# Kernel tuning notes

Hardware: AMD Instinct MI355X
Metric: run time of the kernel (lower is better)

The kernel has to match this reference:

```python
import jax, jax.numpy as jnp
import numpy as np

NEG_SLOPE = 0.2

def gat_layer(x, src, dst, W, a_src, a_dst, num_nodes):
    """PyG-style GATConv. W:[F_in,H*C], a_src/a_dst:[H,C]. Returns [N,H,C]."""
    H, C = a_src.shape
    h = (x @ W).reshape(num_nodes, H, C)                      # [N,H,C]
    e_src = jnp.sum(h * a_src, axis=-1)                       # [N,H]
    e_dst = jnp.sum(h * a_dst, axis=-1)                       # [N,H]
    e = jax.nn.leaky_relu(e_src[src] + e_dst[dst], NEG_SLOPE) # [E,H]
    # segment softmax over incoming edges of each destination node
    m = jax.ops.segment_max(e, dst, num_segments=num_nodes)
    w = jnp.exp(e - m[dst])
    z = jax.ops.segment_sum(w, dst, num_segments=num_nodes)
    alpha = w / (z[dst] + 1e-16)                               # [E,H]
    msg = h[src] * alpha[:, :, None]                           # [E,H,C]
    return jax.ops.segment_sum(msg, dst, num_segments=num_nodes)


def setup_inputs() -> dict:
    key = jax.random.key(0)
    ks = jax.random.split(key, 16)
    N, E, F_IN, HID, A, G = 50000, 800000, 128, 128, 32, 64
    x = jax.random.normal(ks[0], (N, F_IN), dtype=jnp.float32)
    edge_index = jax.random.randint(ks[1], (2, E), 0, N, dtype=jnp.int32)
    batch = jnp.sort(jax.random.randint(ks[2], (N,), 0, G, dtype=jnp.int32))
    s = 0.1
    W1 = jax.random.normal(ks[3], (F_IN, 2 * HID), jnp.float32) * s
    a_src1 = jax.random.normal(ks[4], (2, HID), jnp.float32) * s
    a_dst1 = jax.random.normal(ks[5], (2, HID), jnp.float32) * s
    b1 = jnp.zeros((2 * HID,), jnp.float32)
    W2 = jax.random.normal(ks[6], (2 * HID, HID), jnp.float32) * s
    a_src2 = jax.random.normal(ks[7], (1, HID), jnp.float32) * s
    a_dst2 = jax.random.normal(ks[8], (1, HID), jnp.float32) * s
    b2 = jnp.zeros((HID,), jnp.float32)
    Wp = jax.random.normal(ks[9], (HID, A), jnp.float32) * s
    bp = jnp.zeros((A,), jnp.float32)
    Wv = jax.random.normal(ks[10], (HID, 1), jnp.float32) * s
    bv = jnp.zeros((1,), jnp.float32)
    return {"x": x, "edge_index": edge_index, "batch": batch,
            "W1": W1, "a_src1": a_src1, "a_dst1": a_dst1, "b1": b1,
            "W2": W2, "a_src2": a_src2, "a_dst2": a_dst2, "b2": b2,
            "Wp": Wp, "bp": bp, "Wv": Wv, "bv": bv}


def reference(x, edge_index, batch, W1, a_src1, a_dst1, b1,
              W2, a_src2, a_dst2, b2, Wp, bp, Wv, bv):
    N = x.shape[0]
    G = 64  # number of graphs in the batch
    # add self-loops (PyG GATConv default)
    loop = jnp.arange(N, dtype=edge_index.dtype)
    src = jnp.concatenate([edge_index[0], loop])
    dst = jnp.concatenate([edge_index[1], loop])
    # layer 1: heads=2, concat=True
    h1 = gat_layer(x, src, dst, W1, a_src1, a_dst1, N)        # [N,2,HID]
    h1 = jax.nn.elu(h1.reshape(N, -1) + b1)                   # [N,2*HID]
    # layer 2: heads=1, concat=False (mean over heads = identity for H=1)
    h2 = gat_layer(h1, src, dst, W2, a_src2, a_dst2, N)       # [N,1,HID]
    h2 = jax.nn.elu(h2.reshape(N, -1) + b2)                   # [N,HID]
    # global mean pool over graphs
    sums = jax.ops.segment_sum(h2, batch, num_segments=G)
    cnt = jax.ops.segment_sum(jnp.ones((N,), h2.dtype), batch, num_segments=G)
    x_pool = sums / jnp.maximum(cnt, 1.0)[:, None]            # [G,HID]
    policy_logits = x_pool @ Wp + bp                          # [G,A]
    state_value = x_pool @ Wv + bv                            # [G,1]
    return (policy_logits, state_value)
```

## Files before the change

kernel.cpp:

```cpp
#include <hip/hip_runtime.h>
#include <hip/hip_bf16.h>
#include <cstdint>


typedef __attribute__((ext_vector_type(8))) short bf16x8;
typedef __attribute__((ext_vector_type(4))) float f32x4;

#define RANGES 8

__device__ __forceinline__ float wave_sum(float v) {
#pragma unroll
    for (int off = 32; off >= 1; off >>= 1) v += __shfl_xor(v, off, 64);
    return v;
}

__device__ __forceinline__ unsigned short f2bf(float f) {
    union { float f; uint32_t u; } c; c.f = f;
    uint32_t u = c.u;
    return (unsigned short)((u + 0x7fffu + ((u >> 16) & 1u)) >> 16);
}

__device__ __forceinline__ float bf2f(unsigned short u) {
    union { uint32_t u; float f; } c; c.u = ((uint32_t)u) << 16;
    return c.f;
}


template <int K, int FOUT>
__device__ __forceinline__ void swizzle_body(const float* __restrict__ W, int ldW, int colOff,
                                             unsigned short* __restrict__ Bsw, int tid) {
    constexpr int CPW = FOUT / 4, NCT = CPW / 16, KST = K / 32;
    if (tid >= K * FOUT / 8) return;
    int lane = tid & 63;
    int rest = tid >> 6;
    int t = rest % KST; rest /= KST;
    int c = rest % NCT; rest /= NCT;
    int cg_ = rest;
    int quad = lane >> 4, lo = lane & 15;
    int col = colOff + cg_ * CPW + c * 16 + lo;
    unsigned short v[8];
#pragma unroll
    for (int j = 0; j < 8; ++j)
        v[j] = f2bf(W[(t * 32 + quad * 8 + j) * ldW + col]);
    ushort4* dst = (ushort4*)(Bsw + (size_t)tid * 8);
    ushort4 o0, o1;
    o0.x = v[0]; o0.y = v[1]; o0.z = v[2]; o0.w = v[3];
    o1.x = v[4]; o1.y = v[5]; o1.z = v[6]; o1.w = v[7];
    dst[0] = o0; dst[1] = o1;
}


__global__ void init_kernel(const float* __restrict__ W1, const float* __restrict__ W2,
                            const float* __restrict__ a_src1, const float* __restrict__ a_dst1,
                            unsigned short* __restrict__ B1h0, unsigned short* __restrict__ B1h1,
                            unsigned short* __restrict__ B2,
                            float* __restrict__ v1s, float* __restrict__ v1d,
                            int* __restrict__ zbase, int zn4) {
    int b = blockIdx.x;
    if (b < 8)        swizzle_body<128, 128>(W1, 256, 0,   B1h0, b * 256 + threadIdx.x);
    else if (b < 16)  swizzle_body<128, 128>(W1, 256, 128, B1h1, (b - 8) * 256 + threadIdx.x);
    else if (b < 32)  swizzle_body<256, 128>(W2, 128, 0,   B2, (b - 16) * 256 + threadIdx.x);
    else if (b == 32) {
        int t = threadIdx.x, h = t >> 7, k = t & 127;
        float vs = 0.f, vd = 0.f;
        for (int c = 0; c < 128; ++c) {
            float w = W1[k * 256 + h * 128 + c];
            vs += w * a_src1[h * 128 + c];
            vd += w * a_dst1[h * 128 + c];
        }
        v1s[h * 128 + k] = vs;
        v1d[h * 128 + k] = vd;
    } else {
        int i = (b - 33) * 256 + threadIdx.x;
        if (i < zn4) ((int4*)zbase)[i] = make_int4(0, 0, 0, 0);
    }
}


__global__ void degree_kernel(const int* __restrict__ ei, int* __restrict__ deg,
                              int* __restrict__ eoff, int E, int N) {
    int i = blockIdx.x * blockDim.x + threadIdx.x;
    if (i >= E + N) return;
    int dst = (i < E) ? ei[E + i] : (i - E);
    eoff[i] = atomicAdd(&deg[dst], 1);
}

__global__ __launch_bounds__(256) void scan_tiles(int* __restrict__ deg,
                                                  int* __restrict__ tsum, int N) {
    __shared__ int buf[256];
    const int t = threadIdx.x;
    const int base = blockIdx.x * 1024 + t * 4;
    int v[4]; int s = 0;
#pragma unroll
    for (int k = 0; k < 4; ++k) { v[k] = (base + k < N) ? deg[base + k] : 0; s += v[k]; }
    buf[t] = s;
    __syncthreads();
#pragma unroll
    for (int off = 1; off < 256; off <<= 1) {
        int x = (t >= off) ? buf[t - off] : 0;
        __syncthreads();
        buf[t] += x;
        __syncthreads();
    }
    int run = buf[t] - s;
#pragma unroll
    for (int k = 0; k < 4; ++k) {
        if (base + k < N) deg[base + k] = run;
        run += v[k];
    }
    if (t == 255) tsum[blockIdx.x] = buf[255];
}

__global__ __launch_bounds__(256) void scan_add(const int* __restrict__ partial,
                                                const int* __restrict__ tsum,
                                                int* __restrict__ rowptr, int N, int T) {
    __shared__ int s_toff;
    const int tile = blockIdx.x;
    if (threadIdx.x < 64) {
        int t = threadIdx.x;
        int v = (t < T) ? tsum[t] : 0;
#pragma unroll
        for (int off = 1; off < 64; off <<= 1) {
            int x = __shfl_up(v, off, 64);
            if (t >= off) v += x;
        }
        int toff = (tile == 0) ? 0 : __shfl(v, tile - 1, 64);
        if (t == 0) s_toff = toff;
        if (tile == 0 && t == 63) rowptr[N] = v;
    }
    __syncthreads();
    const int toff = s_toff;
    int i = tile * 1024 + threadIdx.x * 4;
#pragma unroll
    for (int k = 0; k < 4; ++k) {
        if (i + k < N) rowptr[i + k] = partial[i + k] + toff;
    }
}

__global__ void scatter_kernel(const int* __restrict__ ei, const int* __restrict__ eoff,
                               const int* __restrict__ rowptr, int* __restrict__ csr_src,
                               int E, int N, int SBLK, int RSIZE) {
    int r = blockIdx.x / SBLK;
    int i = (blockIdx.x % SBLK) * 256 + threadIdx.x;
    if (i >= E + N) return;
    int dst = (i < E) ? ei[E + i] : (i - E);
    int lo = r * RSIZE;
    if (dst < lo || dst >= lo + RSIZE) return;
    int src = (i < E) ? ei[i] : dst;
    csr_src[rowptr[dst] + eoff[i]] = src;
}


__global__ void attn1_cast(const float* __restrict__ x, const float* __restrict__ v1s,
                           const float* __restrict__ v1d, float* __restrict__ es1,
                           float* __restrict__ ed1, unsigned short* __restrict__ xbf, int N) {
    int wid = (blockIdx.x * blockDim.x + threadIdx.x) >> 6;
    int lane = threadIdx.x & 63;
    if (wid >= N) return;
    float2 xv = *(const float2*)(x + (size_t)wid * 128 + lane * 2);
    float p0s = xv.x * v1s[lane * 2] + xv.y * v1s[lane * 2 + 1];
    float p1s = xv.x * v1s[128 + lane * 2] + xv.y * v1s[128 + lane * 2 + 1];
    float p0d = xv.x * v1d[lane * 2] + xv.y * v1d[lane * 2 + 1];
    float p1d = xv.x * v1d[128 + lane * 2] + xv.y * v1d[128 + lane * 2 + 1];
    p0s = wave_sum(p0s); p1s = wave_sum(p1s);
    p0d = wave_sum(p0d); p1d = wave_sum(p1d);
    if (lane == 0) {
        es1[wid * 2] = p0s; es1[wid * 2 + 1] = p1s;
        ed1[wid * 2] = p0d; ed1[wid * 2 + 1] = p1d;
    }
    ushort2 o; o.x = f2bf(xv.x); o.y = f2bf(xv.y);
    *(ushort2*)(xbf + (size_t)wid * 128 + lane * 2) = o;
}


__global__ void gat_agg_x(const unsigned short* __restrict__ xbf,
                          const float* __restrict__ es, const float* __restrict__ ed,
                          const int* __restrict__ rowptr, const int* __restrict__ csr_src,
                          unsigned short* __restrict__ aggx, int N, int NPAD) {
    __shared__ float w_lds[4][2][32];
    __shared__ int   s_lds[4][32];
    int wid = (blockIdx.x * blockDim.x + threadIdx.x) >> 6;
    int lane = threadIdx.x & 63;
    if (wid >= N) return;
    const int wave = threadIdx.x >> 6;
    const int rs = rowptr[wid], re = rowptr[wid + 1];
    const int half = lane >> 5, c = lane & 31;
    const float edn = ed[wid * 2 + half];

    float z = 0.f;
    float4 a0 = {0.f, 0.f, 0.f, 0.f}, a1 = {0.f, 0.f, 0.f, 0.f};
    float4 a2 = {0.f, 0.f, 0.f, 0.f}, a3 = {0.f, 0.f, 0.f, 0.f};
    for (int i = rs; i < re; i += 32) {
        const int cnt = min(re - i, 32);
        if (c < cnt) {
            int s = csr_src[i + c];
            float e = es[s * 2 + half] + edn;
            e = (e > 0.f) ? e : 0.2f * e;
            float ww = __expf(e);
            w_lds[wave][half][c] = ww;
            if (half == 0) s_lds[wave][c] = s;
            z += ww;
        }
        int k = 0;
        for (; k + 4 <= cnt; k += 4) {
            int s0 = s_lds[wave][k + 0], s1 = s_lds[wave][k + 1];
            int s2 = s_lds[wave][k + 2], s3 = s_lds[wave][k + 3];
            float w0 = w_lds[wave][half][k + 0], w1 = w_lds[wave][half][k + 1];
            float w2 = w_lds[wave][half][k + 2], w3 = w_lds[wave][half][k + 3];
            ushort4 u0 = *(const ushort4*)(xbf + (size_t)s0 * 128 + c * 4);
            ushort4 u1 = *(const ushort4*)(xbf + (size_t)s1 * 128 + c * 4);
            ushort4 u2 = *(const ushort4*)(xbf + (size_t)s2 * 128 + c * 4);
            ushort4 u3 = *(const ushort4*)(xbf + (size_t)s3 * 128 + c * 4);
            a0.x += w0 * bf2f(u0.x); a0.y += w0 * bf2f(u0.y);
            a0.z += w0 * bf2f(u0.z); a0.w += w0 * bf2f(u0.w);
            a1.x += w1 * bf2f(u1.x); a1.y += w1 * bf2f(u1.y);
            a1.z += w1 * bf2f(u1.z); a1.w += w1 * bf2f(u1.w);
            a2.x += w2 * bf2f(u2.x); a2.y += w2 * bf2f(u2.y);
            a2.z += w2 * bf2f(u2.z); a2.w += w2 * bf2f(u2.w);
            a3.x += w3 * bf2f(u3.x); a3.y += w3 * bf2f(u3.y);
            a3.z += w3 * bf2f(u3.z); a3.w += w3 * bf2f(u3.w);
        }
        for (; k < cnt; ++k) {
            int s0 = s_lds[wave][k];
            float w0 = w_lds[wave][half][k];
            ushort4 u0 = *(const ushort4*)(xbf + (size_t)s0 * 128 + c * 4);
            a0.x += w0 * bf2f(u0.x); a0.y += w0 * bf2f(u0.y);
            a0.z += w0 * bf2f(u0.z); a0.w += w0 * bf2f(u0.w);
        }
    }
#pragma unroll
    for (int off = 16; off >= 1; off >>= 1) z += __shfl_xor(z, off, 64);
    const float rz = 1.f / (z + 1e-16f);
    float ox = (a0.x + a1.x + a2.x + a3.x) * rz;
    float oy = (a0.y + a1.y + a2.y + a3.y) * rz;
    float oz = (a0.z + a1.z + a2.z + a3.z) * rz;
    float ow = (a0.w + a1.w + a2.w + a3.w) * rz;
    ushort4 o;
    o.x = f2bf(ox); o.y = f2bf(oy); o.z = f2bf(oz); o.w = f2bf(ow);
    *(ushort4*)(aggx + ((size_t)half * NPAD + wid) * 128 + c * 4) = o;
}


__global__ __launch_bounds__(256) void gemm_plain(const unsigned short* __restrict__ Abase,
                                                  const unsigned short* __restrict__ B0,
                                                  const unsigned short* __restrict__ B1sw,
                                                  const float* __restrict__ bias,
                                                  unsigned short* __restrict__ C,
                                                  int N, int NPAD) {
    constexpr int K = 128, FOUT = 128;
    constexpr int CPW = FOUT / 4, NCT = CPW / 16, KST = K / 32;
    const int head = blockIdx.y;
    const unsigned short* A = Abase + (size_t)head * NPAD * 128;
    const unsigned short* Bsw = head ? B1sw : B0;
    const int colOff = head * 128;
    const int tid = threadIdx.x;
    const int wave = tid >> 6, lane = tid & 63;
    const int quad = lane >> 4, lo = lane & 15;
    const int n0 = blockIdx.x * 64;
    const int c0 = wave * CPW;

    bf16x8 bf[NCT][KST];
    {
        const bf16x8* Bp = (const bf16x8*)Bsw;
#pragma unroll
        for (int c = 0; c < NCT; ++c)
#pragma unroll
            for (int t = 0; t < KST; ++t)
                bf[c][t] = Bp[((wave * NCT + c) * KST + t) * 64 + lane];
    }

    f32x4 acc[4][NCT];
#pragma unroll
    for (int r = 0; r < 4; ++r)
#pragma unroll
        for (int c = 0; c < NCT; ++c) acc[r][c] = (f32x4){0.f, 0.f, 0.f, 0.f};

#pragma unroll
    for (int r = 0; r < 4; ++r) {
        const unsigned short* Ar = A + (size_t)(n0 + r * 16 + lo) * K + quad * 8;
#pragma unroll
        for (int t = 0; t < KST; ++t) {
            bf16x8 af = *(const bf16x8*)(Ar + t * 32);
#pragma unroll
            for (int c = 0; c < NCT; ++c)
                acc[r][c] = __builtin_amdgcn_mfma_f32_16x16x32_bf16(af, bf[c][t], acc[r][c],
                                                                   0, 0, 0);
        }
    }

#pragma unroll
    for (int r = 0; r < 4; ++r) {
        int row = n0 + r * 16 + quad * 4;
#pragma unroll
        for (int c = 0; c < NCT; ++c) {
            int col = colOff + c0 + c * 16 + lo;
            float bv = bias[col];
#pragma unroll
            for (int j = 0; j < 4; ++j) {
                if (row + j < N) {
                    float v = acc[r][c][j] + bv;
                    v = (v > 0.f) ? v : __expf(v) - 1.f;
                    C[(size_t)(row + j) * 256 + col] = f2bf(v);
                }
            }
        }
    }
}


__global__ __launch_bounds__(256) void gemm2_kernel(const unsigned short* __restrict__ A,
                                                    const unsigned short* __restrict__ Bsw,
                                                    const float* __restrict__ a_src,
                                                    const float* __restrict__ a_dst,
                                                    float* __restrict__ es, float* __restrict__ ed,
                                                    unsigned short* __restrict__ C, int N) {
    constexpr int K = 256, FOUT = 128;
    constexpr int CPW = FOUT / 4, NCT = CPW / 16, KST = K / 32;
    const int tid = threadIdx.x;
    const int wave = tid >> 6, lane = tid & 63;
    const int quad = lane >> 4, lo = lane & 15;
    const int n0 = blockIdx.x * 64;
    const int c0 = wave * CPW;
    __shared__ float lds_ps[4][64];
    __shared__ float lds_pd[4][64];

    bf16x8 bf[NCT][KST];
    {
        const bf16x8* Bp = (const bf16x8*)Bsw;
#pragma unroll
        for (int c = 0; c < NCT; ++c)
#pragma unroll
            for (int t = 0; t < KST; ++t)
                bf[c][t] = Bp[((wave * NCT + c) * KST + t) * 64 + lane];
    }

    f32x4 acc[4][NCT];
#pragma unroll
    for (int r = 0; r < 4; ++r)
#pragma unroll
        for (int c = 0; c < NCT; ++c) acc[r][c] = (f32x4){0.f, 0.f, 0.f, 0.f};

#pragma unroll
    for (int r = 0; r < 4; ++r) {
        const unsigned short* Ar = A + (size_t)(n0 + r * 16 + lo) * K + quad * 8;
#pragma unroll
        for (int t = 0; t < KST; ++t) {
            bf16x8 af = *(const bf16x8*)(Ar + t * 32);
#pragma unroll
            for (int c = 0; c < NCT; ++c)
                acc[r][c] = __builtin_amdgcn_mfma_f32_16x16x32_bf16(af, bf[c][t], acc[r][c],
                                                                   0, 0, 0);
        }
    }

#pragma unroll
    for (int r = 0; r < 4; ++r) {
        int row = n0 + r * 16 + quad * 4;
#pragma unroll
        for (int c = 0; c < NCT; ++c) {
            int col = c0 + c * 16 + lo;
#pragma unroll
            for (int j = 0; j < 4; ++j)
                if (row + j < N) C[(size_t)(row + j) * FOUT + col] = f2bf(acc[r][c][j]);
        }
    }

    float asv[NCT], adv[NCT];
#pragma unroll
    for (int c = 0; c < NCT; ++c) {
        int col = c0 + c * 16 + lo;
        asv[c] = a_src[col];
        adv[c] = a_dst[col];
    }
#pragma unroll
    for (int r = 0; r < 4; ++r) {
#pragma unroll
        for (int j = 0; j < 4; ++j) {
            float ps = 0.f, pd = 0.f;
#pragma unroll
            for (int c = 0; c < NCT; ++c) { ps += acc[r][c][j] * asv[c]; pd += acc[r][c][j] * adv[c]; }
#pragma unroll
            for (int off = 1; off <= 8; off <<= 1) {
                ps += __shfl_xor(ps, off, 64);
                pd += __shfl_xor(pd, off, 64);
            }
            if (lo == 0) {
                int row_l = r * 16 + quad * 4 + j;
                lds_ps[wave][row_l] = ps;
                lds_pd[wave][row_l] = pd;
            }
        }
    }
    __syncthreads();
    if (tid < 64) {
        int row = tid;
        int n = n0 + row;
        if (n < N) {
            es[n] = lds_ps[0][row] + lds_ps[1][row] + lds_ps[2][row] + lds_ps[3][row];
            ed[n] = lds_pd[0][row] + lds_pd[1][row] + lds_pd[2][row] + lds_pd[3][row];
        }
    }
}


__global__ void gat_agg_h1(const unsigned short* __restrict__ Hpre,
                           const float* __restrict__ es, const float* __restrict__ ed,
                           const int* __restrict__ rowptr, const int* __restrict__ csr_src,
                           const float* __restrict__ bias, unsigned short* __restrict__ out,
                           int N) {
    __shared__ float w_lds[4][64];
    __shared__ int   s_lds[4][64];
    int wid = (blockIdx.x * blockDim.x + threadIdx.x) >> 6;
    int lane = threadIdx.x & 63;
    if (wid >= N) return;
    const int wave = threadIdx.x >> 6;
    const int rs = rowptr[wid], re = rowptr[wid + 1];
    const int half = lane >> 5, c = lane & 31;
    const float edn = ed[wid];

    float z = 0.f;
    float4 a0 = {0.f, 0.f, 0.f, 0.f}, a1 = {0.f, 0.f, 0.f, 0.f};
    float4 a2 = {0.f, 0.f, 0.f, 0.f}, a3 = {0.f, 0.f, 0.f, 0.f};
    for (int i = rs; i < re; i += 64) {
        const int cnt = min(re - i, 64);
        if (lane < cnt) {
            int s = csr_src[i + lane];
            float e = es[s] + edn;
            e = (e > 0.f) ? e : 0.2f * e;
            float ww = __expf(e);
            w_lds[wave][lane] = ww;
            s_lds[wave][lane] = s;
            z += ww;
        }
        int k = half;
        for (; k + 6 < cnt; k += 8) {
            int s0 = s_lds[wave][k], s1 = s_lds[wave][k + 2];
            int s2 = s_lds[wave][k + 4], s3 = s_lds[wave][k + 6];
            float w0 = w_lds[wave][k], w1 = w_lds[wave][k + 2];
            float w2 = w_lds[wave][k + 4], w3 = w_lds[wave][k + 6];
            ushort4 u0 = *(const ushort4*)(Hpre + (size_t)s0 * 128 + c * 4);
            ushort4 u1 = *(const ushort4*)(Hpre + (size_t)s1 * 128 + c * 4);
            ushort4 u2 = *(const ushort4*)(Hpre + (size_t)s2 * 128 + c * 4);
            ushort4 u3 = *(const ushort4*)(Hpre + (size_t)s3 * 128 + c * 4);
            a0.x += w0 * bf2f(u0.x); a0.y += w0 * bf2f(u0.y);
            a0.z += w0 * bf2f(u0.z); a0.w += w0 * bf2f(u0.w);
            a1.x += w1 * bf2f(u1.x); a1.y += w1 * bf2f(u1.y);
            a1.z += w1 * bf2f(u1.z); a1.w += w1 * bf2f(u1.w);
            a2.x += w2 * bf2f(u2.x); a2.y += w2 * bf2f(u2.y);
            a2.z += w2 * bf2f(u2.z); a2.w += w2 * bf2f(u2.w);
            a3.x += w3 * bf2f(u3.x); a3.y += w3 * bf2f(u3.y);
            a3.z += w3 * bf2f(u3.z); a3.w += w3 * bf2f(u3.w);
        }
        for (; k < cnt; k += 2) {
            int s0 = s_lds[wave][k];
            float w0 = w_lds[wave][k];
            ushort4 u0 = *(const ushort4*)(Hpre + (size_t)s0 * 128 + c * 4);
            a0.x += w0 * bf2f(u0.x); a0.y += w0 * bf2f(u0.y);
            a0.z += w0 * bf2f(u0.z); a0.w += w0 * bf2f(u0.w);
        }
    }
    z = wave_sum(z);
    const float rz = 1.f / (z + 1e-16f);

    float ox = a0.x + a1.x + a2.x + a3.x;
    float oy = a0.y + a1.y + a2.y + a3.y;
    float oz = a0.z + a1.z + a2.z + a3.z;
    float ow = a0.w + a1.w + a2.w + a3.w;
    ox += __shfl_xor(ox, 32, 64);
    oy += __shfl_xor(oy, 32, 64);
    oz += __shfl_xor(oz, 32, 64);
    ow += __shfl_xor(ow, 32, 64);
    if (lane < 32) {
        float4 bv = ((const float4*)bias)[c];
        ox = ox * rz + bv.x; oy = oy * rz + bv.y; oz = oz * rz + bv.z; ow = ow * rz + bv.w;
        ox = (ox > 0.f) ? ox : __expf(ox) - 1.f;
        oy = (oy > 0.f) ? oy : __expf(oy) - 1.f;
        oz = (oz > 0.f) ? oz : __expf(oz) - 1.f;
        ow = (ow > 0.f) ? ow : __expf(ow) - 1.f;
        ushort4 o;
        o.x = f2bf(ox); o.y = f2bf(oy); o.z = f2bf(oz); o.w = f2bf(ow);
        *(ushort4*)(out + (size_t)wid * 128 + c * 4) = o;
    }
}


#define PCHUNK 256

__global__ __launch_bounds__(256) void pool_partial(const unsigned short* __restrict__ h2,
                                                    const int* __restrict__ batch,
                                                    float* __restrict__ xsum,
                                                    int* __restrict__ cnt, int N) {
    const int base = blockIdx.x * PCHUNK;
    const int rg = threadIdx.x >> 6;
    const int c2 = threadIdx.x & 63;
    float ax = 0.f, ay = 0.f;
    int gcur = -1, run = 0;
    for (int r = rg; r < PCHUNK; r += 4) {
        int i = base + r;
        if (i >= N) break;
        int g = batch[i];
        if (g != gcur) {
            if (gcur >= 0) {
                atomicAdd(&xsum[gcur * 128 + c2 * 2 + 0], ax);
                atomicAdd(&xsum[gcur * 128 + c2 * 2 + 1], ay);
                if (c2 == 0) atomicAdd(&cnt[gcur], run);
            }
            gcur = g; ax = 0.f; ay = 0.f; run = 0;
        }
        ushort2 u = *(const ushort2*)(h2 + (size_t)i * 128 + c2 * 2);
        ax += bf2f(u.x); ay += bf2f(u.y);
        run += 1;
    }
    if (gcur >= 0) {
        atomicAdd(&xsum[gcur * 128 + c2 * 2 + 0], ax);
        atomicAdd(&xsum[gcur * 128 + c2 * 2 + 1], ay);
        if (c2 == 0) atomicAdd(&cnt[gcur], run);
    }
}


__global__ void head_kernel(const float* __restrict__ xsum, const int* __restrict__ cnt,
                            const float* __restrict__ Wp, const float* __restrict__ bp,
                            const float* __restrict__ Wv, const float* __restrict__ bv,
                            float* __restrict__ out) {
    int g = blockIdx.x, t = threadIdx.x;
    __shared__ float p[128];
    float inv = 1.f / fmaxf((float)cnt[g], 1.f);
    p[t] = xsum[g * 128 + t] * inv;
    p[t + 64] = xsum[g * 128 + t + 64] * inv;
    __syncthreads();
    if (t < 32) {
        float acc = bp[t];
        for (int k = 0; k < 128; ++k) acc += p[k] * Wp[k * 32 + t];
        out[g * 32 + t] = acc;
    } else if (t == 32) {
        float acc = bv[0];
        for (int k = 0; k < 128; ++k) acc += p[k] * Wv[k];
        out[64 * 32 + g] = acc;
    }
}


extern "C" void kernel_launch(void* const* d_in, const int* in_sizes, int n_in,
                              void* d_out, int out_size, void* d_ws, size_t ws_size,
                              hipStream_t stream) {
    const float* x      = (const float*)d_in[0];
    const int*   ei     = (const int*)d_in[1];
    const int*   batch  = (const int*)d_in[2];
    const float* W1     = (const float*)d_in[3];
    const float* a_src1 = (const float*)d_in[4];
    const float* a_dst1 = (const float*)d_in[5];
    const float* b1     = (const float*)d_in[6];
    const float* W2     = (const float*)d_in[7];
    const float* a_src2 = (const float*)d_in[8];
    const float* a_dst2 = (const float*)d_in[9];
    const float* b2     = (const float*)d_in[10];
    const float* Wp     = (const float*)d_in[11];
    const float* bp     = (const float*)d_in[12];
    const float* Wv     = (const float*)d_in[13];
    const float* bv     = (const float*)d_in[14];

    const int N  = in_sizes[0] / 128;
    const int E  = in_sizes[1] / 2;
    const int ET = E + N;
    const int TILES = (N + 1023) / 1024;
    const int NPAD = ((N + 63) / 64) * 64;
    const int NBLK = NPAD / 64;
    const int SBLK = (ET + 255) / 256;
    const int RSIZE = (N + RANGES - 1) / RANGES;
    const int PBLK = (N + PCHUNK - 1) / PCHUNK;

    char* ws = (char*)d_ws;
    size_t off = 0;
    auto alloc = [&](size_t bytes) -> void* {
        void* p = ws + off;
        off = (off + bytes + 255) & ~(size_t)255;
        return p;
    };
    unsigned short* xbf   = (unsigned short*)alloc((size_t)NPAD * 128 * 2);
    unsigned short* aggx  = (unsigned short*)alloc((size_t)2 * NPAD * 128 * 2);
    unsigned short* h1bf  = (unsigned short*)alloc((size_t)NPAD * 256 * 2);
    unsigned short* h2pre = (unsigned short*)alloc((size_t)NPAD * 128 * 2);
    unsigned short* h2bf  = (unsigned short*)alloc((size_t)N * 128 * 2);
    unsigned short* w1h0  = (unsigned short*)alloc((size_t)128 * 128 * 2);
    unsigned short* w1h1  = (unsigned short*)alloc((size_t)128 * 128 * 2);
    unsigned short* w2sw  = (unsigned short*)alloc((size_t)256 * 128 * 2);
    float* v1s = (float*)alloc(256 * 4);
    float* v1d = (float*)alloc(256 * 4);
    float* es1 = (float*)alloc((size_t)N * 2 * 4);
    float* ed1 = (float*)alloc((size_t)N * 2 * 4);
    float* es2 = (float*)alloc((size_t)N * 4);
    float* ed2 = (float*)alloc((size_t)N * 4);
    const int ZINTS = N + 64 * 128 + 64;
    int*   zbase  = (int*)alloc(((size_t)ZINTS + 8) * 4);
    int*   deg    = zbase;
    float* xsum   = (float*)(zbase + N);
    int*   cnt    = (int*)(xsum + 64 * 128);
    int*   rowptr = (int*)alloc((size_t)(N + 1) * 4);
    int*   eoff   = (int*)alloc((size_t)ET * 4);
    int*   csrsrc = (int*)alloc((size_t)ET * 4);
    int*   tsum   = (int*)alloc(64 * 4);
    const int zn4 = (ZINTS + 3) / 4;

    init_kernel<<<33 + (zn4 + 255) / 256, 256, 0, stream>>>(W1, W2, a_src1, a_dst1,
                                                            w1h0, w1h1, w2sw, v1s, v1d,
                                                            zbase, zn4);

    degree_kernel<<<(ET + 255) / 256, 256, 0, stream>>>(ei, deg, eoff, E, N);
    scan_tiles<<<TILES, 256, 0, stream>>>(deg, tsum, N);
    scan_add<<<TILES, 256, 0, stream>>>(deg, tsum, rowptr, N, TILES);
    scatter_kernel<<<RANGES * SBLK, 256, 0, stream>>>(ei, eoff, rowptr, csrsrc, E, N,
                                                      SBLK, RSIZE);

    attn1_cast<<<(N + 3) / 4, 256, 0, stream>>>(x, v1s, v1d, es1, ed1, xbf, N);
    gat_agg_x<<<(N + 3) / 4, 256, 0, stream>>>(xbf, es1, ed1, rowptr, csrsrc, aggx, N, NPAD);
    gemm_plain<<<dim3(NBLK, 2), 256, 0, stream>>>(aggx, w1h0, w1h1, b1, h1bf, N, NPAD);

    gemm2_kernel<<<NBLK, 256, 0, stream>>>(h1bf, w2sw, a_src2, a_dst2, es2, ed2, h2pre, N);
    gat_agg_h1<<<(N + 3) / 4, 256, 0, stream>>>(h2pre, es2, ed2, rowptr, csrsrc, b2,
                                                h2bf, N);

    pool_partial<<<PBLK, 256, 0, stream>>>(h2bf, batch, xsum, cnt, N);
    head_kernel<<<64, 64, 0, stream>>>(xsum, cnt, Wp, bp, Wv, bv, (float*)d_out);
}
```

Measured before the change: 341.1 us.

## Fuse degree count with attn1 cast, split gather by lane half, deepen unroll

Merges the degree-count kernel and the layer-1 attention/bf16-cast kernel into one launch split by block index, which drops a launch and lets the two independent jobs run side by side. In gat_agg_x, each half-wave now handles alternate edges and accumulates both heads' weights (read as a float2) into two accumulators, combining the halves with a cross-half shuffle at the end. This halves the per-lane edge count and doubles FMAs per load. The layer-2 gather gets an extra 8-wide unrolled loop for more loads in flight, and the scatter range count drops from 8 to 4, so fewer passes over the edge list. The costs are higher register pressure and less locality per scatter pass.

```diff
diff --git a/kernel.cpp b/kernel.cpp
--- a/kernel.cpp
+++ b/kernel.cpp
@@ -6,7 +6,7 @@
 typedef __attribute__((ext_vector_type(8))) short bf16x8;
 typedef __attribute__((ext_vector_type(4))) float f32x4;
 
-#define RANGES 8
+#define RANGES 4
 
 __device__ __forceinline__ float wave_sum(float v) {
 #pragma unroll
@@ -77,84 +77,20 @@
 }
 
 
-__global__ void degree_kernel(const int* __restrict__ ei, int* __restrict__ deg,
-                              int* __restrict__ eoff, int E, int N) {
-    int i = blockIdx.x * blockDim.x + threadIdx.x;
-    if (i >= E + N) return;
-    int dst = (i < E) ? ei[E + i] : (i - E);
-    eoff[i] = atomicAdd(&deg[dst], 1);
-}
-
-__global__ __launch_bounds__(256) void scan_tiles(int* __restrict__ deg,
-                                                  int* __restrict__ tsum, int N) {
-    __shared__ int buf[256];
-    const int t = threadIdx.x;
-    const int base = blockIdx.x * 1024 + t * 4;
-    int v[4]; int s = 0;
-#pragma unroll
-    for (int k = 0; k < 4; ++k) { v[k] = (base + k < N) ? deg[base + k] : 0; s += v[k]; }
-    buf[t] = s;
-    __syncthreads();
-#pragma unroll
-    for (int off = 1; off < 256; off <<= 1) {
-        int x = (t >= off) ? buf[t - off] : 0;
-        __syncthreads();
-        buf[t] += x;
-        __syncthreads();
-    }
-    int run = buf[t] - s;
-#pragma unroll
-    for (int k = 0; k < 4; ++k) {
-        if (base + k < N) deg[base + k] = run;
-        run += v[k];
-    }
-    if (t == 255) tsum[blockIdx.x] = buf[255];
-}
-
-__global__ __launch_bounds__(256) void scan_add(const int* __restrict__ partial,
-                                                const int* __restrict__ tsum,
-                                                int* __restrict__ rowptr, int N, int T) {
-    __shared__ int s_toff;
-    const int tile = blockIdx.x;
-    if (threadIdx.x < 64) {
-        int t = threadIdx.x;
-        int v = (t < T) ? tsum[t] : 0;
-#pragma unroll
-        for (int off = 1; off < 64; off <<= 1) {
-            int x = __shfl_up(v, off, 64);
-            if (t >= off) v += x;
-        }
-        int toff = (tile == 0) ? 0 : __shfl(v, tile - 1, 64);
-        if (t == 0) s_toff = toff;
-        if (tile == 0 && t == 63) rowptr[N] = v;
-    }
-    __syncthreads();
-    const int toff = s_toff;
-    int i = tile * 1024 + threadIdx.x * 4;
-#pragma unroll
-    for (int k = 0; k < 4; ++k) {
-        if (i + k < N) rowptr[i + k] = partial[i + k] + toff;
-    }
-}
-
-__global__ void scatter_kernel(const int* __restrict__ ei, const int* __restrict__ eoff,
-                               const int* __restrict__ rowptr, int* __restrict__ csr_src,
-                               int E, int N, int SBLK, int RSIZE) {
-    int r = blockIdx.x / SBLK;
-    int i = (blockIdx.x % SBLK) * 256 + threadIdx.x;
-    if (i >= E + N) return;
-    int dst = (i < E) ? ei[E + i] : (i - E);
-    int lo = r * RSIZE;
-    if (dst < lo || dst >= lo + RSIZE) return;
-    int src = (i < E) ? ei[i] : dst;
-    csr_src[rowptr[dst] + eoff[i]] = src;
-}
-
-
-__global__ void attn1_cast(const float* __restrict__ x, const float* __restrict__ v1s,
-                           const float* __restrict__ v1d, float* __restrict__ es1,
-                           float* __restrict__ ed1, unsigned short* __restrict__ xbf, int N) {
-    int wid = (blockIdx.x * blockDim.x + threadIdx.x) >> 6;
+__global__ void deg_attn1(const int* __restrict__ ei, int* __restrict__ deg,
+                          int* __restrict__ eoff, int E, int N, int DB,
+                          const float* __restrict__ x, const float* __restrict__ v1s,
+                          const float* __restrict__ v1d, float* __restrict__ es1,
+                          float* __restrict__ ed1, unsigned short* __restrict__ xbf) {
+    if ((int)blockIdx.x < DB) {
+        int i = blockIdx.x * 256 + threadIdx.x;
+        if (i >= E + N) return;
+        int dst = (i < E) ? ei[E + i] : (i - E);
+        eoff[i] = atomicAdd(&deg[dst], 1);
+        return;
+    }
+    int bid = blockIdx.x - DB;
+    int wid = (bid * 256 + threadIdx.x) >> 6;
     int lane = threadIdx.x & 63;
     if (wid >= N) return;
     float2 xv = *(const float2*)(x + (size_t)wid * 128 + lane * 2);
@@ -173,12 +109,84 @@
 }
 
 
+__global__ __launch_bounds__(256) void scan_tiles(int* __restrict__ deg,
+                                                  int* __restrict__ tsum, int N) {
+    __shared__ int buf[256];
+    const int t = threadIdx.x;
+    const int base = blockIdx.x * 1024 + t * 4;
+    int v[4]; int s = 0;
+#pragma unroll
+    for (int k = 0; k < 4; ++k) { v[k] = (base + k < N) ? deg[base + k] : 0; s += v[k]; }
+    buf[t] = s;
+    __syncthreads();
+#pragma unroll
+    for (int off = 1; off < 256; off <<= 1) {
+        int x = (t >= off) ? buf[t - off] : 0;
+        __syncthreads();
+        buf[t] += x;
+        __syncthreads();
+    }
+    int run = buf[t] - s;
+#pragma unroll
+    for (int k = 0; k < 4; ++k) {
+        if (base + k < N) deg[base + k] = run;
+        run += v[k];
+    }
+    if (t == 255) tsum[blockIdx.x] = buf[255];
+}
+
+__global__ __launch_bounds__(256) void scan_add(const int* __restrict__ partial,
+                                                const int* __restrict__ tsum,
+                                                int* __restrict__ rowptr, int N, int T) {
+    __shared__ int s_toff;
+    const int tile = blockIdx.x;
+    if (threadIdx.x < 64) {
+        int t = threadIdx.x;
+        int v = (t < T) ? tsum[t] : 0;
+#pragma unroll
+        for (int off = 1; off < 64; off <<= 1) {
+            int x = __shfl_up(v, off, 64);
+            if (t >= off) v += x;
+        }
+        int toff = (tile == 0) ? 0 : __shfl(v, tile - 1, 64);
+        if (t == 0) s_toff = toff;
+        if (tile == 0 && t == 63) rowptr[N] = v;
+    }
+    __syncthreads();
+    const int toff = s_toff;
+    int i = tile * 1024 + threadIdx.x * 4;
+#pragma unroll
+    for (int k = 0; k < 4; ++k) {
+        if (i + k < N) rowptr[i + k] = partial[i + k] + toff;
+    }
+}
+
+__global__ void scatter_kernel(const int* __restrict__ ei, const int* __restrict__ eoff,
+                               const int* __restrict__ rowptr, int* __restrict__ csr_src,
+                               int E, int N, int SBLK, int RSIZE) {
+    int r = blockIdx.x / SBLK;
+    int i = (blockIdx.x % SBLK) * 256 + threadIdx.x;
+    if (i >= E + N) return;
+    int dst = (i < E) ? ei[E + i] : (i - E);
+    int lo = r * RSIZE;
+    if (dst < lo || dst >= lo + RSIZE) return;
+    int src = (i < E) ? ei[i] : dst;
+    csr_src[rowptr[dst] + eoff[i]] = src;
+}
+
+
+#define ACC2(U_, WW_, P_, Q_) { float v_;                              \
+    v_ = bf2f(U_.x); P_.x += WW_.x * v_; Q_.x += WW_.y * v_;           \
+    v_ = bf2f(U_.y); P_.y += WW_.x * v_; Q_.y += WW_.y * v_;           \
+    v_ = bf2f(U_.z); P_.z += WW_.x * v_; Q_.z += WW_.y * v_;           \
+    v_ = bf2f(U_.w); P_.w += WW_.x * v_; Q_.w += WW_.y * v_; }
+
 __global__ void gat_agg_x(const unsigned short* __restrict__ xbf,
                           const float* __restrict__ es, const float* __restrict__ ed,
                           const int* __restrict__ rowptr, const int* __restrict__ csr_src,
                           unsigned short* __restrict__ aggx, int N, int NPAD) {
-    __shared__ float w_lds[4][2][32];
-    __shared__ int   s_lds[4][32];
+    __shared__ float2 w_lds[4][32];
+    __shared__ int    s_lds[4][32];
     int wid = (blockIdx.x * blockDim.x + threadIdx.x) >> 6;
     int lane = threadIdx.x & 63;
     if (wid >= N) return;
@@ -188,8 +196,8 @@
     const float edn = ed[wid * 2 + half];
 
     float z = 0.f;
-    float4 a0 = {0.f, 0.f, 0.f, 0.f}, a1 = {0.f, 0.f, 0.f, 0.f};
-    float4 a2 = {0.f, 0.f, 0.f, 0.f}, a3 = {0.f, 0.f, 0.f, 0.f};
+    float4 p0 = {0.f, 0.f, 0.f, 0.f}, p1 = {0.f, 0.f, 0.f, 0.f};
+    float4 q0 = {0.f, 0.f, 0.f, 0.f}, q1 = {0.f, 0.f, 0.f, 0.f};
     for (int i = rs; i < re; i += 32) {
         const int cnt = min(re - i, 32);
         if (c < cnt) {
@@ -197,44 +205,46 @@
             float e = es[s * 2 + half] + edn;
             e = (e > 0.f) ? e : 0.2f * e;
             float ww = __expf(e);
-            w_lds[wave][half][c] = ww;
+            ((float*)&w_lds[wave][c])[half] = ww;
             if (half == 0) s_lds[wave][c] = s;
             z += ww;
         }
-        int k = 0;
-        for (; k + 4 <= cnt; k += 4) {
-            int s0 = s_lds[wave][k + 0], s1 = s_lds[wave][k + 1];
-            int s2 = s_lds[wave][k + 2], s3 = s_lds[wave][k + 3];
-            float w0 = w_lds[wave][half][k + 0], w1 = w_lds[wave][half][k + 1];
-            float w2 = w_lds[wave][half][k + 2], w3 = w_lds[wave][half][k + 3];
+        int k = half;
+        for (; k + 6 < cnt; k += 8) {
+            int s0 = s_lds[wave][k + 0], s1 = s_lds[wave][k + 2];
+            int s2 = s_lds[wave][k + 4], s3 = s_lds[wave][k + 6];
+            float2 wv0 = w_lds[wave][k + 0], wv1 = w_lds[wave][k + 2];
+            float2 wv2 = w_lds[wave][k + 4], wv3 = w_lds[wave][k + 6];
             ushort4 u0 = *(const ushort4*)(xbf + (size_t)s0 * 128 + c * 4);
             ushort4 u1 = *(const ushort4*)(xbf + (size_t)s1 * 128 + c * 4);
             ushort4 u2 = *(const ushort4*)(xbf + (size_t)s2 * 128 + c * 4);
             ushort4 u3 = *(const ushort4*)(xbf + (size_t)s3 * 128 + c * 4);
-            a0.x += w0 * bf2f(u0.x); a0.y += w0 * bf2f(u0.y);
-            a0.z += w0 * bf2f(u0.z); a0.w += w0 * bf2f(u0.w);
-            a1.x += w1 * bf2f(u1.x); a1.y += w1 * bf2f(u1.y);
-            a1.z += w1 * bf2f(u1.z); a1.w += w1 * bf2f(u1.w);
-            a2.x += w2 * bf2f(u2.x); a2.y += w2 * bf2f(u2.y);
-            a2.z += w2 * bf2f(u2.z); a2.w += w2 * bf2f(u2.w);
-            a3.x += w3 * bf2f(u3.x); a3.y += w3 * bf2f(u3.y);
-            a3.z += w3 * bf2f(u3.z); a3.w += w3 * bf2f(u3.w);
-        }
-        for (; k < cnt; ++k) {
+            ACC2(u0, wv0, p0, q0);
+            ACC2(u1, wv1, p1, q1);
+            ACC2(u2, wv2, p0, q0);
+            ACC2(u3, wv3, p1, q1);
+        }
+        for (; k < cnt; k += 2) {
             int s0 = s_lds[wave][k];
-            float w0 = w_lds[wave][half][k];
+            float2 wv = w_lds[wave][k];
             ushort4 u0 = *(const ushort4*)(xbf + (size_t)s0 * 128 + c * 4);
-            a0.x += w0 * bf2f(u0.x); a0.y += w0 * bf2f(u0.y);
-            a0.z += w0 * bf2f(u0.z); a0.w += w0 * bf2f(u0.w);
+            ACC2(u0, wv, p0, q0);
         }
     }
 #pragma unroll
     for (int off = 16; off >= 1; off >>= 1) z += __shfl_xor(z, off, 64);
     const float rz = 1.f / (z + 1e-16f);
-    float ox = (a0.x + a1.x + a2.x + a3.x) * rz;
-    float oy = (a0.y + a1.y + a2.y + a3.y) * rz;
-    float oz = (a0.z + a1.z + a2.z + a3.z) * rz;
-    float ow = (a0.w + a1.w + a2.w + a3.w) * rz;
+    float4 p, q;
+    p.x = p0.x + p1.x; p.y = p0.y + p1.y; p.z = p0.z + p1.z; p.w = p0.w + p1.w;
+    q.x = q0.x + q1.x; q.y = q0.y + q1.y; q.z = q0.z + q1.z; q.w = q0.w + q1.w;
+    p.x += __shfl_xor(p.x, 32, 64); p.y += __shfl_xor(p.y, 32, 64);
+    p.z += __shfl_xor(p.z, 32, 64); p.w += __shfl_xor(p.w, 32, 64);
+    q.x += __shfl_xor(q.x, 32, 64); q.y += __shfl_xor(q.y, 32, 64);
+    q.z += __shfl_xor(q.z, 32, 64); q.w += __shfl_xor(q.w, 32, 64);
+    float ox = (half ? q.x : p.x) * rz;
+    float oy = (half ? q.y : p.y) * rz;
+    float oz = (half ? q.z : p.z) * rz;
+    float ow = (half ? q.w : p.w) * rz;
     ushort4 o;
     o.x = f2bf(ox); o.y = f2bf(oy); o.z = f2bf(oz); o.w = f2bf(ow);
     *(ushort4*)(aggx + ((size_t)half * NPAD + wid) * 128 + c * 4) = o;
@@ -433,6 +443,40 @@
             z += ww;
         }
         int k = half;
+        for (; k + 14 < cnt; k += 16) {
+            int s0 = s_lds[wave][k],      s1 = s_lds[wave][k + 2];
+            int s2 = s_lds[wave][k + 4],  s3 = s_lds[wave][k + 6];
+            int s4 = s_lds[wave][k + 8],  s5 = s_lds[wave][k + 10];
+            int s6 = s_lds[wave][k + 12], s7 = s_lds[wave][k + 14];
+            float w0 = w_lds[wave][k],      w1 = w_lds[wave][k + 2];
+            float w2 = w_lds[wave][k + 4],  w3 = w_lds[wave][k + 6];
+            float w4 = w_lds[wave][k + 8],  w5 = w_lds[wave][k + 10];
+            float w6 = w_lds[wave][k + 12], w7 = w_lds[wave][k + 14];
+            ushort4 u0 = *(const ushort4*)(Hpre + (size_t)s0 * 128 + c * 4);
+            ushort4 u1 = *(const ushort4*)(Hpre + (size_t)s1 * 128 + c * 4);
+            ushort4 u2 = *(const ushort4*)(Hpre + (size_t)s2 * 128 + c * 4);
+            ushort4 u3 = *(const ushort4*)(Hpre + (size_t)s3 * 128 + c * 4);
+            ushort4 u4 = *(const ushort4*)(Hpre + (size_t)s4 * 128 + c * 4);
+            ushort4 u5 = *(const ushort4*)(Hpre + (size_t)s5 * 128 + c * 4);
+            ushort4 u6 = *(const ushort4*)(Hpre + (size_t)s6 * 128 + c * 4);
+            ushort4 u7 = *(const ushort4*)(Hpre + (size_t)s7 * 128 + c * 4);
+            a0.x += w0 * bf2f(u0.x); a0.y += w0 * bf2f(u0.y);
+            a0.z += w0 * bf2f(u0.z); a0.w += w0 * bf2f(u0.w);
+            a1.x += w1 * bf2f(u1.x); a1.y += w1 * bf2f(u1.y);
+            a1.z += w1 * bf2f(u1.z); a1.w += w1 * bf2f(u1.w);
+            a2.x += w2 * bf2f(u2.x); a2.y += w2 * bf2f(u2.y);
+            a2.z += w2 * bf2f(u2.z); a2.w += w2 * bf2f(u2.w);
+            a3.x += w3 * bf2f(u3.x); a3.y += w3 * bf2f(u3.y);
+            a3.z += w3 * bf2f(u3.z); a3.w += w3 * bf2f(u3.w);
+            a0.x += w4 * bf2f(u4.x); a0.y += w4 * bf2f(u4.y);
+            a0.z += w4 * bf2f(u4.z); a0.w += w4 * bf2f(u4.w);
+            a1.x += w5 * bf2f(u5.x); a1.y += w5 * bf2f(u5.y);
+            a1.z += w5 * bf2f(u5.z); a1.w += w5 * bf2f(u5.w);
+            a2.x += w6 * bf2f(u6.x); a2.y += w6 * bf2f(u6.y);
+            a2.z += w6 * bf2f(u6.z); a2.w += w6 * bf2f(u6.w);
+            a3.x += w7 * bf2f(u7.x); a3.y += w7 * bf2f(u7.y);
+            a3.z += w7 * bf2f(u7.z); a3.w += w7 * bf2f(u7.w);
+        }
         for (; k + 6 < cnt; k += 8) {
             int s0 = s_lds[wave][k], s1 = s_lds[wave][k + 2];
             int s2 = s_lds[wave][k + 4], s3 = s_lds[wave][k + 6];
@@ -569,6 +613,8 @@
     const int SBLK = (ET + 255) / 256;
     const int RSIZE = (N + RANGES - 1) / RANGES;
     const int PBLK = (N + PCHUNK - 1) / PCHUNK;
+    const int DB = (ET + 255) / 256;
+    const int AB = (N + 3) / 4;
 
     char* ws = (char*)d_ws;
     size_t off = 0;
@@ -606,13 +652,14 @@
                                                             w1h0, w1h1, w2sw, v1s, v1d,
                                                             zbase, zn4);
 
-    degree_kernel<<<(ET + 255) / 256, 256, 0, stream>>>(ei, deg, eoff, E, N);
+    deg_attn1<<<DB + AB, 256, 0, stream>>>(ei, deg, eoff, E, N, DB,
+                                           x, v1s, v1d, es1, ed1, xbf);
+
     scan_tiles<<<TILES, 256, 0, stream>>>(deg, tsum, N);
     scan_add<<<TILES, 256, 0, stream>>>(deg, tsum, rowptr, N, TILES);
     scatter_kernel<<<RANGES * SBLK, 256, 0, stream>>>(ei, eoff, rowptr, csrsrc, E, N,
                                                       SBLK, RSIZE);
 
-    attn1_cast<<<(N + 3) / 4, 256, 0, stream>>>(x, v1s, v1d, es1, ed1, xbf, N);
     gat_agg_x<<<(N + 3) / 4, 256, 0, stream>>>(xbf, es1, ed1, rowptr, csrsrc, aggx, N, NPAD);
     gemm_plain<<<dim3(NBLK, 2), 256, 0, stream>>>(aggx, w1h0, w1h1, b1, h1bf, N, NPAD);
 
```

After: 329.3 us. -3.5%, faster.
